# Optimization experiments

Measured on AMD Instinct MI355X. Metric: run time of the kernel, lower is better.

Reference implementation:

```python
import jax, jax.numpy as jnp
import numpy as np

KNOTS = 17

def _buffers(dtype=jnp.float32):
    t = jnp.linspace(0.0, 3.0, KNOTS, dtype=dtype)
    dt = 3.0 / (KNOTS - 1)
    w = jnp.full((KNOTS,), 2.0 * dt, dtype=dtype).at[0].set(dt).at[-1].set(dt)
    phi = jnp.exp(-jnp.square(t) / 2.0)
    return t, phi, w * phi


def setup_inputs() -> dict:
    key = jax.random.key(0)
    k1, k2 = jax.random.split(key)
    T, B, D, P = 32, 64, 256, 1024
    proj = jax.random.normal(k1, (T, B, D), dtype=jnp.float32)
    A = jax.random.normal(k2, (D, P), dtype=jnp.float32)
    return {"proj": proj, "A": A}


def reference(proj, A):
    t, phi, weights = _buffers(proj.dtype)
    # column-normalize random projection directions (matches A.div_(norm.clamp_min))
    A = A / jnp.maximum(jnp.linalg.norm(A, axis=0, keepdims=True), 1e-12)
    B = proj.shape[-2]
    # (T, B, P) projections, broadcast against knots -> (T, B, P, K)
    x_t = (proj @ A)[..., None] * t
    # empirical characteristic function averaged over batch dim B (dim -3)
    cos_mean = jnp.cos(x_t).mean(axis=-3)  # (T, P, K)
    sin_mean = jnp.sin(x_t).mean(axis=-3)  # (T, P, K)
    err = jnp.square(cos_mean - phi) + jnp.square(sin_mean)
    statistic = (err @ weights) * B  # (T, P)
    return statistic.mean()
```

## Files before the change

kernel.cpp:

```cpp
#include <hip/hip_runtime.h>

#define T_DIM 32
#define B_DIM 64
#define D_DIM 256
#define P_DIM 1024
#define NK    17
#define DT    0.1875f

#define KC    128
#define LROW  136

typedef __bf16 bf16x8 __attribute__((ext_vector_type(8)));
typedef float  f32x16 __attribute__((ext_vector_type(16)));

static __device__ __forceinline__ unsigned f2bf(float f) {
  unsigned u = __float_as_uint(f);
  u += 0x7fffu + ((u >> 16) & 1u);
  return u >> 16;
}

__global__ __launch_bounds__(256) void sig_fused_kernel(const float* __restrict__ proj,
                                                        const float* __restrict__ A,
                                                        float* __restrict__ out) {
  __shared__ float smf[9792];
  unsigned short* sp = (unsigned short*)smf;
  unsigned short* sa = sp + 64 * LROW;
  float* normred = smf + 8704;
  float* invn    = smf + 9728;

  const int tid  = threadIdx.x;
  const int lane = tid & 63;
  const int wv   = tid >> 6;
  const int p0   = blockIdx.x * 64;
  const int t    = blockIdx.y;

  const int mt = wv >> 1, nt = wv & 1;
  const int mrow = mt * 32 + (lane & 31);
  const int nrow = nt * 32 + (lane & 31);
  const int koff = (lane >> 5) * 8;

  const float4* Pg = (const float4*)(proj + (size_t)t * B_DIM * D_DIM);
  const float4* Ag = (const float4*)(A + p0);

  const int pg = tid & 15;
  const int dg = tid >> 4;

  f32x16 acc = {0.f, 0.f, 0.f, 0.f, 0.f, 0.f, 0.f, 0.f,
                0.f, 0.f, 0.f, 0.f, 0.f, 0.f, 0.f, 0.f};
  float nrm[4] = {0.f, 0.f, 0.f, 0.f};

  for (int kc = 0; kc < D_DIM; kc += KC) {
#pragma unroll
    for (int r = 0; r < 4; ++r) {
      int pair = tid + r * 256;
      int row = pair >> 4, cp = pair & 15;
      float4 v0 = Pg[row * 64 + kc / 4 + cp * 2];
      float4 v1 = Pg[row * 64 + kc / 4 + cp * 2 + 1];
      uint4 w;
      w.x = f2bf(v0.x) | (f2bf(v0.y) << 16);
      w.y = f2bf(v0.z) | (f2bf(v0.w) << 16);
      w.z = f2bf(v1.x) | (f2bf(v1.y) << 16);
      w.w = f2bf(v1.z) | (f2bf(v1.w) << 16);
      *(uint4*)&sp[row * LROW + cp * 8] = w;
    }
    {
      float4 va[8];
#pragma unroll
      for (int i = 0; i < 8; ++i)
        va[i] = Ag[(size_t)(kc + dg * 8 + i) * (P_DIM / 4) + pg];
#pragma unroll
      for (int j = 0; j < 4; ++j) {
        float e0 = ((const float*)&va[0])[j], e1 = ((const float*)&va[1])[j];
        float e2 = ((const float*)&va[2])[j], e3 = ((const float*)&va[3])[j];
        float e4 = ((const float*)&va[4])[j], e5 = ((const float*)&va[5])[j];
        float e6 = ((const float*)&va[6])[j], e7 = ((const float*)&va[7])[j];
        nrm[j] = fmaf(e0, e0, nrm[j]); nrm[j] = fmaf(e1, e1, nrm[j]);
        nrm[j] = fmaf(e2, e2, nrm[j]); nrm[j] = fmaf(e3, e3, nrm[j]);
        nrm[j] = fmaf(e4, e4, nrm[j]); nrm[j] = fmaf(e5, e5, nrm[j]);
        nrm[j] = fmaf(e6, e6, nrm[j]); nrm[j] = fmaf(e7, e7, nrm[j]);
        uint4 w;
        w.x = f2bf(e0) | (f2bf(e1) << 16);
        w.y = f2bf(e2) | (f2bf(e3) << 16);
        w.z = f2bf(e4) | (f2bf(e5) << 16);
        w.w = f2bf(e6) | (f2bf(e7) << 16);
        *(uint4*)&sa[(pg * 4 + j) * LROW + dg * 8] = w;
      }
    }
    if (kc != 0) {
#pragma unroll
      for (int j = 0; j < 4; ++j) normred[dg * 64 + pg * 4 + j] = nrm[j];
    }
    __syncthreads();

#pragma unroll
    for (int ks = 0; ks < 8; ++ks) {
      int k = ks * 16 + koff;
      bf16x8 af = *(const bf16x8*)&sp[mrow * LROW + k];
      bf16x8 bf = *(const bf16x8*)&sa[nrow * LROW + k];
      acc = __builtin_amdgcn_mfma_f32_32x32x16_bf16(af, bf, acc, 0, 0, 0);
    }
    __syncthreads();
  }

  if (tid < 64) {
    float s = 0.f;
#pragma unroll
    for (int q = 0; q < 16; ++q) s += normred[q * 64 + tid];
    invn[tid] = rsqrtf(fmaxf(s, 1e-24f));
  }
  __syncthreads();
  const float invdt = invn[nt * 32 + (lane & 31)] * DT;

  float cs[NK - 1], ss[NK - 1];
#pragma unroll
  for (int k = 0; k < NK - 1; ++k) { cs[k] = 0.f; ss[k] = 0.f; }
#pragma unroll
  for (int r = 0; r < 16; ++r) {
    float th = acc[r] * invdt;
    float s1, c1;
    __sincosf(th, &s1, &c1);
    float twoc = 2.f * c1;
    float ckm1 = 1.f, skm1 = 0.f;
    float ck = c1, sk = s1;
    cs[0] += c1;
    ss[0] += s1;
#pragma unroll
    for (int k = 2; k < NK; ++k) {
      float cn = fmaf(twoc, ck, -ckm1);
      float sn = fmaf(twoc, sk, -skm1);
      cs[k - 1] += cn;
      ss[k - 1] += sn;
      ckm1 = ck; skm1 = sk; ck = cn; sk = sn;
    }
  }

#pragma unroll
  for (int k = 0; k < NK - 1; ++k) {
    cs[k] += __shfl_xor(cs[k], 32, 64);
    ss[k] += __shfl_xor(ss[k], 32, 64);
  }

  if (lane < 32) {
    int p = nt * 32 + (lane & 31);
#pragma unroll
    for (int k = 0; k < NK - 1; ++k) {
      smf[k * 128 + mt * 64 + p]        = cs[k];
      smf[2048 + k * 128 + mt * 64 + p] = ss[k];
    }
  }
  __syncthreads();

  float part = 0.f;
#pragma unroll
  for (int r = 0; r < 4; ++r) {
    int e  = tid + r * 256;
    int k1 = e >> 6;
    int pl = e & 63;
    float C = smf[k1 * 128 + pl] + smf[k1 * 128 + 64 + pl];
    float S = smf[2048 + k1 * 128 + pl] + smf[2048 + k1 * 128 + 64 + pl];
    float cm  = C * (1.f / 64.f);
    float sm_ = S * (1.f / 64.f);
    float tk  = (float)(k1 + 1) * DT;
    float phi = __expf(-0.5f * tk * tk);
    float wk  = ((k1 == NK - 2) ? DT : 2.f * DT) * phi;
    float dc  = cm - phi;
    part = fmaf(wk, fmaf(dc, dc, sm_ * sm_), part);
  }
  part *= (1.f / 512.f);

#pragma unroll
  for (int off = 32; off > 0; off >>= 1)
    part += __shfl_down(part, off, 64);
  __syncthreads();
  if (lane == 0) smf[4096 + wv] = part;
  __syncthreads();
  if (tid == 0)
    atomicAdd(out, smf[4096] + smf[4097] + smf[4098] + smf[4099]);
}

extern "C" void kernel_launch(void* const* d_in, const int* in_sizes, int n_in,
                              void* d_out, int out_size, void* d_ws, size_t ws_size,
                              hipStream_t stream) {
  const float* proj = (const float*)d_in[0];
  const float* A    = (const float*)d_in[1];
  float* out        = (float*)d_out;

  hipMemsetAsync(out, 0, sizeof(float), stream);
  sig_fused_kernel<<<dim3(16, 32), dim3(256), 0, stream>>>(proj, A, out);
}
```

Before: 70.26 us.

## Double block to 512 threads using 16x16x32 MFMA tiles per wave

Each block now runs 8 waves instead of 4. Every wave computes a 16x32 output slab with two 16x16x32 bf16 MFMAs in place of one 32x32x16 tile. The tail (sincos recurrence and per-knot sums) is therefore spread over twice as many threads, which shortens the serial per-thread trig work, and the global loads are split across more threads. In exchange it adds extra shuffle reductions, more LDS traffic for the four-way partial sums, and an additional barrier cost with more waves.

After: 71.72 us. 2.1% more time.

```diff
diff --git a/kernel.cpp b/kernel.cpp
--- a/kernel.cpp
+++ b/kernel.cpp
@@ -11,7 +11,7 @@
 #define LROW  136
 
 typedef __bf16 bf16x8 __attribute__((ext_vector_type(8)));
-typedef float  f32x16 __attribute__((ext_vector_type(16)));
+typedef float  f32x4  __attribute__((ext_vector_type(4)));
 
 static __device__ __forceinline__ unsigned f2bf(float f) {
   unsigned u = __float_as_uint(f);
@@ -19,41 +19,46 @@
   return u >> 16;
 }
 
-__global__ __launch_bounds__(256) void sig_fused_kernel(const float* __restrict__ proj,
-                                                        const float* __restrict__ A,
-                                                        float* __restrict__ out) {
-  __shared__ float smf[9792];
+__global__ __launch_bounds__(512, 4) void sig_fused_kernel(const float* __restrict__ proj,
+                                                           const float* __restrict__ A,
+                                                           float* __restrict__ out) {
+  __shared__ float smf[10816];
   unsigned short* sp = (unsigned short*)smf;
   unsigned short* sa = sp + 64 * LROW;
   float* normred = smf + 8704;
-  float* invn    = smf + 9728;
+  float* invn    = smf + 10752;
 
   const int tid  = threadIdx.x;
   const int lane = tid & 63;
   const int wv   = tid >> 6;
+  const int mq   = wv >> 1;
+  const int nh   = wv & 1;
   const int p0   = blockIdx.x * 64;
   const int t    = blockIdx.y;
 
-  const int mt = wv >> 1, nt = wv & 1;
-  const int mrow = mt * 32 + (lane & 31);
-  const int nrow = nt * 32 + (lane & 31);
-  const int koff = (lane >> 5) * 8;
-
   const float4* Pg = (const float4*)(proj + (size_t)t * B_DIM * D_DIM);
   const float4* Ag = (const float4*)(A + p0);
 
-  const int pg = tid & 15;
-  const int dg = tid >> 4;
-
-  f32x16 acc = {0.f, 0.f, 0.f, 0.f, 0.f, 0.f, 0.f, 0.f,
-                0.f, 0.f, 0.f, 0.f, 0.f, 0.f, 0.f, 0.f};
+  const int pg  = tid & 15;
+  const int dgq = tid >> 4;
+
+  const int l15 = lane & 15;
+  const int mrow  = mq * 16 + l15;
+  const int prow0 = nh * 32 + l15;
+  const int prow1 = prow0 + 16;
+  const int kq    = (lane >> 4) * 8;
+
+  f32x4 acc0 = {0.f, 0.f, 0.f, 0.f};
+  f32x4 acc1 = {0.f, 0.f, 0.f, 0.f};
   float nrm[4] = {0.f, 0.f, 0.f, 0.f};
 
-  for (int kc = 0; kc < D_DIM; kc += KC) {
-#pragma unroll
-    for (int r = 0; r < 4; ++r) {
-      int pair = tid + r * 256;
-      int row = pair >> 4, cp = pair & 15;
+#pragma unroll
+  for (int c = 0; c < 2; ++c) {
+    const int kc = c * KC;
+#pragma unroll
+    for (int r = 0; r < 2; ++r) {
+      int idx = tid + r * 512;
+      int row = idx >> 4, cp = idx & 15;
       float4 v0 = Pg[row * 64 + kc / 4 + cp * 2];
       float4 v1 = Pg[row * 64 + kc / 4 + cp * 2 + 1];
       uint4 w;
@@ -64,40 +69,38 @@
       *(uint4*)&sp[row * LROW + cp * 8] = w;
     }
     {
-      float4 va[8];
-#pragma unroll
-      for (int i = 0; i < 8; ++i)
-        va[i] = Ag[(size_t)(kc + dg * 8 + i) * (P_DIM / 4) + pg];
+      float4 va[4];
+#pragma unroll
+      for (int i = 0; i < 4; ++i)
+        va[i] = Ag[(size_t)(kc + dgq * 4 + i) * (P_DIM / 4) + pg];
 #pragma unroll
       for (int j = 0; j < 4; ++j) {
-        float e0 = ((const float*)&va[0])[j], e1 = ((const float*)&va[1])[j];
-        float e2 = ((const float*)&va[2])[j], e3 = ((const float*)&va[3])[j];
-        float e4 = ((const float*)&va[4])[j], e5 = ((const float*)&va[5])[j];
-        float e6 = ((const float*)&va[6])[j], e7 = ((const float*)&va[7])[j];
+        float e0 = ((const float*)&va[0])[j];
+        float e1 = ((const float*)&va[1])[j];
+        float e2 = ((const float*)&va[2])[j];
+        float e3 = ((const float*)&va[3])[j];
         nrm[j] = fmaf(e0, e0, nrm[j]); nrm[j] = fmaf(e1, e1, nrm[j]);
         nrm[j] = fmaf(e2, e2, nrm[j]); nrm[j] = fmaf(e3, e3, nrm[j]);
-        nrm[j] = fmaf(e4, e4, nrm[j]); nrm[j] = fmaf(e5, e5, nrm[j]);
-        nrm[j] = fmaf(e6, e6, nrm[j]); nrm[j] = fmaf(e7, e7, nrm[j]);
-        uint4 w;
+        uint2 w;
         w.x = f2bf(e0) | (f2bf(e1) << 16);
         w.y = f2bf(e2) | (f2bf(e3) << 16);
-        w.z = f2bf(e4) | (f2bf(e5) << 16);
-        w.w = f2bf(e6) | (f2bf(e7) << 16);
-        *(uint4*)&sa[(pg * 4 + j) * LROW + dg * 8] = w;
+        *(uint2*)&sa[(pg * 4 + j) * LROW + dgq * 4] = w;
       }
     }
-    if (kc != 0) {
-#pragma unroll
-      for (int j = 0; j < 4; ++j) normred[dg * 64 + pg * 4 + j] = nrm[j];
+    if (c == 1) {
+#pragma unroll
+      for (int j = 0; j < 4; ++j) normred[dgq * 64 + pg * 4 + j] = nrm[j];
     }
     __syncthreads();
 
 #pragma unroll
-    for (int ks = 0; ks < 8; ++ks) {
-      int k = ks * 16 + koff;
-      bf16x8 af = *(const bf16x8*)&sp[mrow * LROW + k];
-      bf16x8 bf = *(const bf16x8*)&sa[nrow * LROW + k];
-      acc = __builtin_amdgcn_mfma_f32_32x32x16_bf16(af, bf, acc, 0, 0, 0);
+    for (int ks = 0; ks < 4; ++ks) {
+      int kb = ks * 32 + kq;
+      bf16x8 af = *(const bf16x8*)&sp[mrow * LROW + kb];
+      bf16x8 b0 = *(const bf16x8*)&sa[prow0 * LROW + kb];
+      bf16x8 b1 = *(const bf16x8*)&sa[prow1 * LROW + kb];
+      acc0 = __builtin_amdgcn_mfma_f32_16x16x32_bf16(af, b0, acc0, 0, 0, 0);
+      acc1 = __builtin_amdgcn_mfma_f32_16x16x32_bf16(af, b1, acc1, 0, 0, 0);
     }
     __syncthreads();
   }
@@ -105,59 +108,67 @@
   if (tid < 64) {
     float s = 0.f;
 #pragma unroll
-    for (int q = 0; q < 16; ++q) s += normred[q * 64 + tid];
+    for (int q = 0; q < 32; ++q) s += normred[q * 64 + tid];
     invn[tid] = rsqrtf(fmaxf(s, 1e-24f));
   }
   __syncthreads();
-  const float invdt = invn[nt * 32 + (lane & 31)] * DT;
-
-  float cs[NK - 1], ss[NK - 1];
-#pragma unroll
-  for (int k = 0; k < NK - 1; ++k) { cs[k] = 0.f; ss[k] = 0.f; }
-#pragma unroll
-  for (int r = 0; r < 16; ++r) {
-    float th = acc[r] * invdt;
-    float s1, c1;
-    __sincosf(th, &s1, &c1);
-    float twoc = 2.f * c1;
-    float ckm1 = 1.f, skm1 = 0.f;
-    float ck = c1, sk = s1;
-    cs[0] += c1;
-    ss[0] += s1;
-#pragma unroll
-    for (int k = 2; k < NK; ++k) {
-      float cn = fmaf(twoc, ck, -ckm1);
-      float sn = fmaf(twoc, sk, -skm1);
-      cs[k - 1] += cn;
-      ss[k - 1] += sn;
-      ckm1 = ck; skm1 = sk; ck = cn; sk = sn;
-    }
-  }
-
-#pragma unroll
-  for (int k = 0; k < NK - 1; ++k) {
-    cs[k] += __shfl_xor(cs[k], 32, 64);
-    ss[k] += __shfl_xor(ss[k], 32, 64);
-  }
-
-  if (lane < 32) {
-    int p = nt * 32 + (lane & 31);
+
+#pragma unroll
+  for (int nt = 0; nt < 2; ++nt) {
+    const f32x4 a = nt ? acc1 : acc0;
+    const int   p = nh * 32 + nt * 16 + l15;
+    const float invdt = invn[p] * DT;
+    float cs[NK - 1], ss[NK - 1];
+#pragma unroll
+    for (int k = 0; k < NK - 1; ++k) { cs[k] = 0.f; ss[k] = 0.f; }
+#pragma unroll
+    for (int r = 0; r < 4; ++r) {
+      float th = a[r] * invdt;
+      float s1, c1;
+      __sincosf(th, &s1, &c1);
+      float twoc = 2.f * c1;
+      float ckm1 = 1.f, skm1 = 0.f;
+      float ck = c1, sk = s1;
+      cs[0] += c1;
+      ss[0] += s1;
+#pragma unroll
+      for (int k = 2; k < NK; ++k) {
+        float cn = fmaf(twoc, ck, -ckm1);
+        float sn = fmaf(twoc, sk, -skm1);
+        cs[k - 1] += cn;
+        ss[k - 1] += sn;
+        ckm1 = ck; skm1 = sk; ck = cn; sk = sn;
+      }
+    }
 #pragma unroll
     for (int k = 0; k < NK - 1; ++k) {
-      smf[k * 128 + mt * 64 + p]        = cs[k];
-      smf[2048 + k * 128 + mt * 64 + p] = ss[k];
+      cs[k] += __shfl_xor(cs[k], 16, 64);
+      cs[k] += __shfl_xor(cs[k], 32, 64);
+      ss[k] += __shfl_xor(ss[k], 16, 64);
+      ss[k] += __shfl_xor(ss[k], 32, 64);
+    }
+    if (lane < 16) {
+#pragma unroll
+      for (int k = 0; k < NK - 1; ++k) {
+        smf[k * 256 + mq * 64 + p]        = cs[k];
+        smf[4096 + k * 256 + mq * 64 + p] = ss[k];
+      }
     }
   }
   __syncthreads();
 
   float part = 0.f;
 #pragma unroll
-  for (int r = 0; r < 4; ++r) {
-    int e  = tid + r * 256;
+  for (int r = 0; r < 2; ++r) {
+    int e  = tid + r * 512;
     int k1 = e >> 6;
     int pl = e & 63;
-    float C = smf[k1 * 128 + pl] + smf[k1 * 128 + 64 + pl];
-    float S = smf[2048 + k1 * 128 + pl] + smf[2048 + k1 * 128 + 64 + pl];
+    float C = 0.f, S = 0.f;
+#pragma unroll
+    for (int m = 0; m < 4; ++m) {
+      C += smf[k1 * 256 + m * 64 + pl];
+      S += smf[4096 + k1 * 256 + m * 64 + pl];
+    }
     float cm  = C * (1.f / 64.f);
     float sm_ = S * (1.f / 64.f);
     float tk  = (float)(k1 + 1) * DT;
@@ -171,11 +182,14 @@
 #pragma unroll
   for (int off = 32; off > 0; off >>= 1)
     part += __shfl_down(part, off, 64);
+  if (lane == 0) smf[8192 + wv] = part;
   __syncthreads();
-  if (lane == 0) smf[4096 + wv] = part;
-  __syncthreads();
-  if (tid == 0)
-    atomicAdd(out, smf[4096] + smf[4097] + smf[4098] + smf[4099]);
+  if (tid == 0) {
+    float s = 0.f;
+#pragma unroll
+    for (int w = 0; w < 8; ++w) s += smf[8192 + w];
+    atomicAdd(out, s);
+  }
 }
 
 extern "C" void kernel_launch(void* const* d_in, const int* in_sizes, int n_in,
@@ -186,5 +200,5 @@
   float* out        = (float*)d_out;
 
   hipMemsetAsync(out, 0, sizeof(float), stream);
-  sig_fused_kernel<<<dim3(16, 32), dim3(256), 0, stream>>>(proj, A, out);
+  sig_fused_kernel<<<dim3(16, 32), dim3(512), 0, stream>>>(proj, A, out);
 }
```
